# Kernel tuning notes

Hardware: AMD Instinct MI355X
Metric: run time of the kernel (lower is better)

Reference implementation:

```python
import jax, jax.numpy as jnp
import numpy as np
from jax import lax

K = 9
ISHAPE = (2048, 2048)
STRIDES = (4, 8, 16, 32)
NUM_ROIS = 300
IOU_THR = 0.5
SCORE_THR = 0.5
PRE_NMS_TOPK = 4000  # standard pre-NMS candidate cap; keeps suppression loop small


def _make_anchors(h, w, stride):
    scales = np.array([1.0, 2.0, 4.0]) * 4.0 * stride
    ratios = np.sqrt(np.array([0.5, 1.0, 2.0]))
    ah = (scales[:, None] * ratios[None, :]).reshape(-1)   # (9,)
    aw = (scales[:, None] / ratios[None, :]).reshape(-1)
    cy = (np.arange(h, dtype=np.float32) + 0.5) * stride
    cx = (np.arange(w, dtype=np.float32) + 0.5) * stride
    cy, cx = np.meshgrid(cy, cx, indexing='ij')             # (h,w)
    y1 = cy[..., None] - 0.5 * ah
    x1 = cx[..., None] - 0.5 * aw
    y2 = cy[..., None] + 0.5 * ah
    x2 = cx[..., None] + 0.5 * aw
    return np.stack([y1, x1, y2, x2], axis=-1).astype(np.float32)  # (h,w,9,4)


def setup_inputs() -> dict:
    key = jax.random.key(0)
    ks = jax.random.split(key, 4)
    sizes = [(512, 512), (256, 256), (128, 128), (64, 64)]
    out = {}
    for i, ((h, w), s, k) in enumerate(zip(sizes, STRIDES, ks), start=1):
        out[f'x{i}'] = jax.random.uniform(k, (1, h, w, 6 * K), dtype=jnp.float32)
        out[f'anchors{i}'] = jnp.asarray(_make_anchors(h, w, s))
    return out


def _decode_level(clzbbe, anchors):
    # clzbbe: (h,w,6k) -> (h,w,k,6); channels per anchor: [fg, bg, dy, dx, dh, dw]
    h, w, k, _ = anchors.shape
    t = clzbbe.reshape(h, w, k, 6)
    scores = t[..., 0]
    dy, dx, dh, dw = t[..., 2], t[..., 3], t[..., 4], t[..., 5]
    ah = anchors[..., 2] - anchors[..., 0]
    aw = anchors[..., 3] - anchors[..., 1]
    acy = anchors[..., 0] + 0.5 * ah
    acx = anchors[..., 1] + 0.5 * aw
    cy = acy + dy * ah
    cx = acx + dx * aw
    bh = ah * jnp.exp(dh)
    bw = aw * jnp.exp(dw)
    y1 = jnp.clip(cy - 0.5 * bh, 0.0, float(ISHAPE[0]))
    x1 = jnp.clip(cx - 0.5 * bw, 0.0, float(ISHAPE[1]))
    y2 = jnp.clip(cy + 0.5 * bh, 0.0, float(ISHAPE[0]))
    x2 = jnp.clip(cx + 0.5 * bw, 0.0, float(ISHAPE[1]))
    boxes = jnp.stack([y1, x1, y2, x2], axis=-1).reshape(-1, 4)
    return boxes, scores.reshape(-1)


def _iou_one_vs_all(box, boxes):
    yy1 = jnp.maximum(box[0], boxes[:, 0])
    xx1 = jnp.maximum(box[1], boxes[:, 1])
    yy2 = jnp.minimum(box[2], boxes[:, 2])
    xx2 = jnp.minimum(box[3], boxes[:, 3])
    inter = jnp.maximum(yy2 - yy1, 0.0) * jnp.maximum(xx2 - xx1, 0.0)
    a1 = (box[2] - box[0]) * (box[3] - box[1])
    a2 = (boxes[:, 2] - boxes[:, 0]) * (boxes[:, 3] - boxes[:, 1])
    return inter / (a1 + a2 - inter + 1e-9)


def _pnsm(boxes, scores):
    # pre-NMS top-k candidates
    top_scores, top_idx = lax.top_k(scores, PRE_NMS_TOPK)
    cand_boxes = boxes[top_idx]                              # (TOPK, 4)
    s0 = jnp.where(top_scores >= SCORE_THR, top_scores, -1.0)

    def step(s, _):
        i = jnp.argmax(s)
        best_score = s[i]
        best_box = cand_boxes[i]
        iou = _iou_one_vs_all(best_box, cand_boxes)
        s = jnp.where(iou > IOU_THR, -1.0, s).at[i].set(-1.0)
        roi = jnp.where(best_score > 0.0, best_box, jnp.zeros_like(best_box))
        return s, roi

    _, rois = lax.scan(step, s0, None, length=NUM_ROIS)      # (NUM_ROIS, 4)
    return rois


def reference(x1, x2, x3, x4, anchors1, anchors2, anchors3, anchors4):
    levels = [(x1[0], anchors1), (x2[0], anchors2), (x3[0], anchors3), (x4[0], anchors4)]
    decoded = [_decode_level(c, a) for c, a in levels]
    boxes = jnp.concatenate([b for b, _ in decoded], axis=0)   # (N, 4)
    scores = jnp.concatenate([s for _, s in decoded], axis=0)  # (N,)
    rois = _pnsm(boxes, scores)
    return rois[None]                                          # (1, NUM_ROIS, 4)
```

## Files before the change

kernel.cpp:

```cpp
#include <hip/hip_runtime.h>


namespace {

constexpr int kNTot = 3133440;
constexpr int kB1 = 2359296;
constexpr int kB2 = 2949120;
constexpr int kB3 = 3096576;
constexpr int kNBins = 8192;
constexpr int kNParts = 256;
constexpr int kCap = 8192;
constexpr int kTopK = 4000;
constexpr int kNPad = 4096;
constexpr int kNRois = 300;
constexpr int kChunk = 32;
constexpr int kNChunks = kTopK / kChunk;
constexpr int kNSlots = 8;
constexpr int kNPref = 7;
constexpr int kJChunk = 2048;
constexpr int kITile = 256;
constexpr int kBCS = 16;

constexpr int kF4L[4] = {3538944, 884736, 221184, 55296};
constexpr int kLvlB0[5] = {0, 193, 241, 253, 256};
constexpr int kLvlAB[4] = {0, kB1, kB2, kB3};

struct LevelPick { const float* x; unsigned local; };

__device__ __forceinline__ LevelPick pick_level(unsigned g, const float* x1, const float* x2,
                                                const float* x3, const float* x4) {
  LevelPick p;
  if (g < (unsigned)kB1)      { p.x = x1; p.local = g; }
  else if (g < (unsigned)kB2) { p.x = x2; p.local = g - kB1; }
  else if (g < (unsigned)kB3) { p.x = x3; p.local = g - kB2; }
  else                        { p.x = x4; p.local = g - kB3; }
  return p;
}

__device__ __forceinline__ int score_bin(float s) {
  int b = (int)(s * (float)kNBins);
  return min(max(b, 0), kNBins - 1);
}

__device__ __forceinline__ void load_scores4(const float* x, unsigned local0, float s[4]) {
  const float4* p = (const float4*)(x + (size_t)local0 * 6);
  float4 q0 = p[0], q1 = p[1], q3 = p[3], q4 = p[4];
  s[0] = q0.x; s[1] = q1.z; s[2] = q3.x; s[3] = q4.z;
}

__global__ __launch_bounds__(1024) void hist_kernel(
    const float4* __restrict__ x1, const float4* __restrict__ x2,
    const float4* __restrict__ x3, const float4* __restrict__ x4,
    unsigned* __restrict__ part, float* __restrict__ scores) {
  __shared__ unsigned h[kNBins];
  for (int i = threadIdx.x; i < kNBins; i += 1024) h[i] = 0;
  __syncthreads();
  const int bid = blockIdx.x;
  int lvl = (bid < kLvlB0[1]) ? 0 : (bid < kLvlB0[2]) ? 1 : (bid < kLvlB0[3]) ? 2 : 3;
  const float4* x = (lvl == 0) ? x1 : (lvl == 1) ? x2 : (lvl == 2) ? x3 : x4;
  const int nf4 = kF4L[lvl];
  const int abase = kLvlAB[lvl];
  const int bloc = bid - kLvlB0[lvl];
  const int nblk = kLvlB0[lvl + 1] - kLvlB0[lvl];
  for (int q = bloc * 1024 + threadIdx.x; q < nf4; q += nblk * 1024) {
    float4 v = x[q];
    int qd = q / 3;
    int r = q - qd * 3;
    if (r != 2) {
      float s = (r == 0) ? v.x : v.z;
      atomicAdd(&h[score_bin(s)], 1u);
      if (scores) scores[abase + 2 * qd + r] = s;
    }
  }
  __syncthreads();
  for (int i = threadIdx.x; i < kNBins; i += 1024)
    part[blockIdx.x * kNBins + i] = h[i];
}

__global__ void reduce_kernel(const unsigned* __restrict__ part, unsigned* __restrict__ hist) {
  int b = blockIdx.x * 256 + threadIdx.x;
  unsigned t0 = 0, t1 = 0, t2 = 0, t3 = 0;
  for (int p = 0; p < kNParts; p += 4) {
    t0 += part[(size_t)(p + 0) * kNBins + b];
    t1 += part[(size_t)(p + 1) * kNBins + b];
    t2 += part[(size_t)(p + 2) * kNBins + b];
    t3 += part[(size_t)(p + 3) * kNBins + b];
  }
  hist[b] = t0 + t1 + t2 + t3;
}

__global__ __launch_bounds__(1024) void select_kernel(
    const unsigned* __restrict__ hist, unsigned* __restrict__ sel,
    unsigned* __restrict__ counter, unsigned* __restrict__ binStart) {
  __shared__ unsigned wtot[16];
  __shared__ unsigned maxB;
  const int t = threadIdx.x;
  const int lane = t & 63;
  const int wv = t >> 6;
  if (t == 0) maxB = 0u;
  unsigned h[8];
  unsigned s = 0;
  #pragma unroll
  for (int i = 0; i < 8; ++i) { h[i] = hist[t * 8 + i]; s += h[i]; }
  unsigned p = s;
  #pragma unroll
  for (int off = 1; off < 64; off <<= 1) {
    unsigned n = __shfl_up(p, off);
    if (lane >= off) p += n;
  }
  if (lane == 63) wtot[wv] = p;
  __syncthreads();
  if (wv == 0 && lane < 16) {
    unsigned wp = wtot[lane];
    #pragma unroll
    for (int off = 1; off < 16; off <<= 1) {
      unsigned n = __shfl_up(wp, off);
      if (lane >= off) wp += n;
    }
    wtot[lane] = wp;
  }
  __syncthreads();
  const unsigned total = wtot[15];
  const unsigned Pincl = p + (wv > 0 ? wtot[wv - 1] : 0u);
  const unsigned T = total - Pincl;
  unsigned bs[8];
  bs[7] = T;
  #pragma unroll
  for (int i = 6; i >= 0; --i) bs[i] = bs[i + 1] + h[i + 1];
  #pragma unroll
  for (int i = 0; i < 8; ++i) binStart[t * 8 + i] = bs[i];
  unsigned cand = 0;
  #pragma unroll
  for (int i = 0; i < 8; ++i)
    if (bs[i] + h[i] >= (unsigned)kTopK) cand = (unsigned)(t * 8 + i);
  atomicMax(&maxB, cand);
  __syncthreads();
  const unsigned B = maxB;
  if (t == (int)(B >> 3)) {
    unsigned i = B & 7u;
    unsigned n = bs[i] + h[i];
    sel[0] = B;
    counter[0] = n < (unsigned)kCap ? n : (unsigned)kCap;
  }
}

__device__ __forceinline__ void try_append(float s, unsigned g, unsigned B,
                                           const unsigned* __restrict__ binStart,
                                           unsigned* __restrict__ binCount,
                                           unsigned long long* __restrict__ keys) {
  unsigned bin = (unsigned)score_bin(s);
  if (bin >= B) {
    unsigned pos = binStart[bin] + atomicAdd(&binCount[bin << 4], 1u);
    if (pos < (unsigned)kCap) {
      keys[pos] = ((unsigned long long)__float_as_uint(s) << 32) |
                  (unsigned long long)(0xFFFFFFFFu - g);
    }
  }
}

__global__ void compact_s_kernel(const float4* __restrict__ scores4,
                                 const unsigned* __restrict__ sel,
                                 const unsigned* __restrict__ binStart,
                                 unsigned* __restrict__ binCount,
                                 unsigned long long* __restrict__ keys) {
  int t = blockIdx.x * blockDim.x + threadIdx.x;
  if (t >= kNTot / 4) return;
  float4 v = scores4[t];
  unsigned g0 = (unsigned)t * 4;
  unsigned B = sel[0];
  try_append(v.x, g0 + 0, B, binStart, binCount, keys);
  try_append(v.y, g0 + 1, B, binStart, binCount, keys);
  try_append(v.z, g0 + 2, B, binStart, binCount, keys);
  try_append(v.w, g0 + 3, B, binStart, binCount, keys);
}

__global__ void compact_x_kernel(const float* __restrict__ x1, const float* __restrict__ x2,
                                 const float* __restrict__ x3, const float* __restrict__ x4,
                                 const unsigned* __restrict__ sel,
                                 const unsigned* __restrict__ binStart,
                                 unsigned* __restrict__ binCount,
                                 unsigned long long* __restrict__ keys) {
  int t = blockIdx.x * blockDim.x + threadIdx.x;
  if (t >= kNTot / 4) return;
  unsigned g0 = (unsigned)t * 4;
  LevelPick lp = pick_level(g0, x1, x2, x3, x4);
  float s[4];
  load_scores4(lp.x, lp.local, s);
  unsigned B = sel[0];
  #pragma unroll
  for (int i = 0; i < 4; ++i) try_append(s[i], g0 + i, B, binStart, binCount, keys);
}

__global__ void rank_kernel(const unsigned long long* __restrict__ keys,
                            const unsigned* __restrict__ counter,
                            unsigned* __restrict__ rankArr) {
  __shared__ unsigned long long lk[kJChunk];
  int n = (int)*counter;
  int itile = blockIdx.x / (kCap / kJChunk);
  int jc = blockIdx.x % (kCap / kJChunk);
  int i0 = itile * kITile;
  int j0 = jc * kJChunk;
  if (i0 >= n || j0 >= n) return;
  for (int j = threadIdx.x; j < kJChunk; j += kITile) {
    int jj = j0 + j;
    lk[j] = (jj < n) ? keys[jj] : 0ull;
  }
  __syncthreads();
  int i = i0 + threadIdx.x;
  unsigned long long ki = (i < n) ? keys[i] : ~0ull;
  int r0 = 0, r1 = 0, r2 = 0, r3 = 0;
  const ulonglong2* p2 = (const ulonglong2*)lk;
  #pragma unroll 4
  for (int j = 0; j < kJChunk / 8; ++j) {
    ulonglong2 a = p2[j];
    ulonglong2 b = p2[256 + j];
    ulonglong2 c = p2[512 + j];
    ulonglong2 d = p2[768 + j];
    r0 += (int)(a.x > ki) + (int)(a.y > ki);
    r1 += (int)(b.x > ki) + (int)(b.y > ki);
    r2 += (int)(c.x > ki) + (int)(c.y > ki);
    r3 += (int)(d.x > ki) + (int)(d.y > ki);
  }
  if (i < n) atomicAdd(&rankArr[i], (unsigned)(r0 + r1 + r2 + r3));
}

__global__ void scatter_kernel(const unsigned long long* __restrict__ keys,
                               const unsigned* __restrict__ counter,
                               const unsigned* __restrict__ rankArr,
                               unsigned long long* __restrict__ sorted) {
  int i = blockIdx.x * 256 + threadIdx.x;
  int n = (int)*counter;
  if (i < n) {
    unsigned r = rankArr[i];
    if (r < (unsigned)kNPad) sorted[r] = keys[i];
  }
}

__device__ __forceinline__ void decode_box(unsigned g,
                                           const float* __restrict__ x1, const float* __restrict__ x2,
                                           const float* __restrict__ x3, const float* __restrict__ x4,
                                           const float* __restrict__ a1, const float* __restrict__ a2,
                                           const float* __restrict__ a3, const float* __restrict__ a4,
                                           float4* box) {
  const float* x;
  const float* anc;
  unsigned local;
  if (g < (unsigned)kB1)      { x = x1; anc = a1; local = g; }
  else if (g < (unsigned)kB2) { x = x2; anc = a2; local = g - kB1; }
  else if (g < (unsigned)kB3) { x = x3; anc = a3; local = g - kB2; }
  else                        { x = x4; anc = a4; local = g - kB3; }
  const float* xe = x + (size_t)local * 6;
  float dy = xe[2], dx = xe[3], dh = xe[4], dwv = xe[5];
  const float* ae = anc + (size_t)local * 4;
  float ay1 = ae[0], ax1 = ae[1], ay2 = ae[2], ax2 = ae[3];
  float ah = ay2 - ay1;
  float aw = ax2 - ax1;
  float acy = ay1 + 0.5f * ah;
  float acx = ax1 + 0.5f * aw;
  float cy = acy + dy * ah;
  float cx = acx + dx * aw;
  float bh = ah * expf(dh);
  float bw = aw * expf(dwv);
  box->x = fminf(fmaxf(cy - 0.5f * bh, 0.0f), 2048.0f);
  box->y = fminf(fmaxf(cx - 0.5f * bw, 0.0f), 2048.0f);
  box->z = fminf(fmaxf(cy + 0.5f * bh, 0.0f), 2048.0f);
  box->w = fminf(fmaxf(cx + 0.5f * bw, 0.0f), 2048.0f);
}

__global__ void decode_kernel(const unsigned long long* __restrict__ sorted,
                              const unsigned* __restrict__ counter,
                              const float* __restrict__ x1, const float* __restrict__ x2,
                              const float* __restrict__ x3, const float* __restrict__ x4,
                              const float* __restrict__ a1, const float* __restrict__ a2,
                              const float* __restrict__ a3, const float* __restrict__ a4,
                              float4* __restrict__ boxes,
                              unsigned long long* __restrict__ supinit) {
  int r = blockIdx.x * 256 + threadIdx.x;
  int n = min((int)*counter, kTopK);
  unsigned long long key = (r < n) ? sorted[r] : 0ull;
  float4 box = make_float4(0.f, 0.f, 0.f, 0.f);
  float sc = 0.f;
  if (key != 0ull) {
    sc = __uint_as_float((unsigned)(key >> 32));
    unsigned g = 0xFFFFFFFFu - (unsigned)(key & 0xFFFFFFFFull);
    if (g < (unsigned)kNTot) decode_box(g, x1, x2, x3, x4, a1, a2, a3, a4, &box);
  }
  boxes[r] = box;
  unsigned long long dead = __ballot(!(sc >= 0.5f));
  if ((threadIdx.x & 63) == 0) supinit[r >> 6] = dead;
}

__global__ void iou_kernel(const float4* __restrict__ boxes,
                           unsigned long long* __restrict__ rows) {
  int wave = (blockIdx.x * blockDim.x + threadIdx.x) >> 6;
  int lane = threadIdx.x & 63;
  if (wave >= kTopK * 64) return;
  int row = wave >> 6;
  int wc = wave & 63;
  if (wc < (row >> 6)) return;
  int j = wc * 64 + lane;
  float4 bi = boxes[row];
  float4 bj = boxes[j];
  float yy1 = fmaxf(bi.x, bj.x);
  float xx1 = fmaxf(bi.y, bj.y);
  float yy2 = fminf(bi.z, bj.z);
  float xx2 = fminf(bi.w, bj.w);
  float inter = fmaxf(yy2 - yy1, 0.0f) * fmaxf(xx2 - xx1, 0.0f);
  float ar1 = (bi.z - bi.x) * (bi.w - bi.y);
  float ar2 = (bj.z - bj.x) * (bj.w - bj.y);
  float iou = inter / (ar1 + ar2 - inter + 1e-9f);
  unsigned long long m = __ballot(iou > 0.5f);
  if (lane == 0) rows[(size_t)row * 64 + wc] = m;
}

__device__ __forceinline__ void glds16(const void* g, void* l) {
  __builtin_amdgcn_global_load_lds(
      (const __attribute__((address_space(1))) unsigned int*)g,
      (__attribute__((address_space(3))) unsigned int*)l, 16, 0, 0);
}

__device__ __forceinline__ void stage_chunk(const unsigned long long* rows, int chunk,
                                            unsigned long long* dst, int lane) {
  const char* src = (const char*)(rows + (size_t)chunk * kChunk * 64);
  char* d = (char*)dst;
  #pragma unroll
  for (int i = 0; i < 16; ++i) {
    glds16(src + i * 1024 + lane * 16, d + i * 1024);
  }
}

__global__ __launch_bounds__(512, 1) void greedy_kernel(
    const float4* __restrict__ boxes,
    const unsigned long long* __restrict__ supinit,
    const unsigned long long* __restrict__ rows,
    float* __restrict__ out) {
  __shared__ unsigned long long slots[kNSlots][kChunk * 64];
  __shared__ unsigned readyF[kNChunks];
  __shared__ unsigned consumedF;
  __shared__ unsigned doneF;
  __shared__ int picksLds[kNRois];
  __shared__ int countSh;

  volatile unsigned* vready = readyF;
  volatile unsigned* vconsumed = &consumedF;
  volatile unsigned* vdone = &doneF;

  const int tid = threadIdx.x;
  const int wid = tid >> 6;
  const int lane = tid & 63;

  for (int i = tid; i < kNChunks; i += 512) readyF[i] = 0;
  if (tid == 0) { consumedF = 0; doneF = 0; countSh = 0; }
  __syncthreads();

  if (wid > 0) {
    int c = wid - 1;
    bool primed = false;
    if (c < kNChunks) {
      while (!*vdone && (int)*vconsumed < c - (kNSlots - 1))
        __builtin_amdgcn_s_sleep(1);
      if (!*vdone) {
        stage_chunk(rows, c, &slots[c & (kNSlots - 1)][0], lane);
        primed = true;
      }
    }
    while (primed) {
      int nxt = c + kNPref;
      bool staged_next = false;
      if (nxt < kNChunks) {
        while (!*vdone && (int)*vconsumed < nxt - (kNSlots - 1))
          __builtin_amdgcn_s_sleep(1);
        if (!*vdone) {
          stage_chunk(rows, nxt, &slots[nxt & (kNSlots - 1)][0], lane);
          staged_next = true;
        }
      }
      if (staged_next) {
        asm volatile("s_waitcnt vmcnt(16)" ::: "memory");
      } else {
        asm volatile("s_waitcnt vmcnt(0)" ::: "memory");
      }
      if (lane == 0) vready[c] = 1;
      if (!staged_next) break;
      c = nxt;
    }
  } else {
    unsigned long long sup = supinit[lane];
    int count = 0;
    for (int c = 0; c < kNChunks; ++c) {
      while (vready[c] == 0) __builtin_amdgcn_s_sleep(1);
      asm volatile("" ::: "memory");
      const unsigned long long* buf = &slots[c & (kNSlots - 1)][0];
      const int base = c * kChunk;
      const int w = base >> 6;
      const int sh = base & 63;
      unsigned long long cw = __shfl(sup, w);
      unsigned mask = (unsigned)((~cw) >> sh);
      while (mask != 0u && count < kNRois) {
        const int i = __builtin_ctz(mask);
        const int r = base + i;
        unsigned long long row = buf[i * 64 + lane];
        if (lane == 0) picksLds[count] = r;
        ++count;
        sup |= row;
        if (lane == w) sup |= 1ull << (r & 63);
        unsigned long long rww = __shfl(row, w);
        mask &= ~(unsigned)(rww >> sh);
        mask &= ~(1u << i);
      }
      if (lane == 0) *vconsumed = (unsigned)(c + 1);
      if (count == kNRois) break;
      if (__ballot(~sup != 0ull) == 0ull) break;
    }
    if (lane == 0) { countSh = count; *vdone = 1u; }
  }
  __syncthreads();
  const int cnt = countSh;
  for (int p = tid; p < kNRois; p += 512) {
    float4 bx = make_float4(0.f, 0.f, 0.f, 0.f);
    if (p < cnt) bx = boxes[picksLds[p]];
    ((float4*)out)[p] = bx;
  }
}

}

extern "C" void kernel_launch(void* const* d_in, const int* in_sizes, int n_in,
                              void* d_out, int out_size, void* d_ws, size_t ws_size,
                              hipStream_t stream) {
  const float* x1 = (const float*)d_in[0];
  const float* a1 = (const float*)d_in[1];
  const float* x2 = (const float*)d_in[2];
  const float* a2 = (const float*)d_in[3];
  const float* x3 = (const float*)d_in[4];
  const float* a3 = (const float*)d_in[5];
  const float* x4 = (const float*)d_in[6];
  const float* a4 = (const float*)d_in[7];

  char* ws = (char*)d_ws;
  size_t off = 0;
  unsigned* part = (unsigned*)(ws + off);       off += (size_t)kNParts * kNBins * 4;
  unsigned* hist = (unsigned*)(ws + off);       off += kNBins * 4;
  unsigned* counter = (unsigned*)(ws + off);    off += 4;
  unsigned* sel = (unsigned*)(ws + off);        off += 4;
  unsigned* rankArr = (unsigned*)(ws + off);    off += (size_t)kCap * 4;
  unsigned* binCount = (unsigned*)(ws + off);   off += (size_t)kNBins * kBCS * 4;
  unsigned* binStart = (unsigned*)(ws + off);   off += (size_t)kNBins * 4;
  unsigned long long* supinit = (unsigned long long*)(ws + off);  off += 512 + 8;
  unsigned long long* sorted = (unsigned long long*)(ws + off);   off += (size_t)kNPad * 8;
  unsigned long long* keys = (unsigned long long*)(ws + off);     off += (size_t)kCap * 8;
  float4* boxes = (float4*)(ws + off);          off += (size_t)kNPad * 16;
  unsigned long long* rows = (unsigned long long*)(ws + off);     off += (size_t)kTopK * 64 * 8;
  const bool sidecar = ws_size >= off + (size_t)kNTot * 4;
  float* scores = sidecar ? (float*)(ws + off) : nullptr;
  float* out = (float*)d_out;

  hipMemsetAsync((void*)counter, 0, 8 + (size_t)kCap * 4 + (size_t)kNBins * kBCS * 4,
                 stream);

  hist_kernel<<<kNParts, 1024, 0, stream>>>(
      (const float4*)x1, (const float4*)x2, (const float4*)x3, (const float4*)x4,
      part, scores);
  reduce_kernel<<<kNBins / 256, 256, 0, stream>>>(part, hist);
  select_kernel<<<1, 1024, 0, stream>>>(hist, sel, counter, binStart);
  int blocks4 = (kNTot / 4 + 255) / 256;
  if (sidecar) {
    compact_s_kernel<<<blocks4, 256, 0, stream>>>(
        (const float4*)scores, sel, binStart, binCount, keys);
  } else {
    compact_x_kernel<<<blocks4, 256, 0, stream>>>(
        x1, x2, x3, x4, sel, binStart, binCount, keys);
  }
  rank_kernel<<<(kCap / kITile) * (kCap / kJChunk), kITile, 0, stream>>>(
      keys, counter, rankArr);
  scatter_kernel<<<kCap / 256, 256, 0, stream>>>(keys, counter, rankArr, sorted);
  decode_kernel<<<kNPad / 256, 256, 0, stream>>>(
      sorted, counter, x1, x2, x3, x4, a1, a2, a3, a4, boxes, supinit);
  iou_kernel<<<(kTopK * 64 * 64) / 256, 256, 0, stream>>>(boxes, rows);
  greedy_kernel<<<1, 512, 0, stream>>>(boxes, supinit, rows, out);
}
```

Before: 139.2 us.

## Replace producer-consumer LDS staging in greedy NMS with sparse alive-row register prefetch

```diff
diff --git a/kernel.cpp b/kernel.cpp
--- a/kernel.cpp
+++ b/kernel.cpp
@@ -13,10 +13,6 @@
 constexpr int kTopK = 4000;
 constexpr int kNPad = 4096;
 constexpr int kNRois = 300;
-constexpr int kChunk = 32;
-constexpr int kNChunks = kTopK / kChunk;
-constexpr int kNSlots = 8;
-constexpr int kNPref = 7;
 constexpr int kJChunk = 2048;
 constexpr int kITile = 256;
 constexpr int kBCS = 16;
@@ -313,112 +309,85 @@
   if (lane == 0) rows[(size_t)row * 64 + wc] = m;
 }
 
-__device__ __forceinline__ void glds16(const void* g, void* l) {
-  __builtin_amdgcn_global_load_lds(
-      (const __attribute__((address_space(1))) unsigned int*)g,
-      (__attribute__((address_space(3))) unsigned int*)l, 16, 0, 0);
-}
-
-__device__ __forceinline__ void stage_chunk(const unsigned long long* rows, int chunk,
-                                            unsigned long long* dst, int lane) {
-  const char* src = (const char*)(rows + (size_t)chunk * kChunk * 64);
-  char* d = (char*)dst;
-  #pragma unroll
-  for (int i = 0; i < 16; ++i) {
-    glds16(src + i * 1024 + lane * 16, d + i * 1024);
-  }
-}
-
-__global__ __launch_bounds__(512, 1) void greedy_kernel(
+__global__ __launch_bounds__(64, 1) void greedy_kernel(
     const float4* __restrict__ boxes,
     const unsigned long long* __restrict__ supinit,
     const unsigned long long* __restrict__ rows,
     float* __restrict__ out) {
-  __shared__ unsigned long long slots[kNSlots][kChunk * 64];
-  __shared__ unsigned readyF[kNChunks];
-  __shared__ unsigned consumedF;
-  __shared__ unsigned doneF;
   __shared__ int picksLds[kNRois];
-  __shared__ int countSh;
-
-  volatile unsigned* vready = readyF;
-  volatile unsigned* vconsumed = &consumedF;
-  volatile unsigned* vdone = &doneF;
-
-  const int tid = threadIdx.x;
-  const int wid = tid >> 6;
-  const int lane = tid & 63;
-
-  for (int i = tid; i < kNChunks; i += 512) readyF[i] = 0;
-  if (tid == 0) { consumedF = 0; doneF = 0; countSh = 0; }
-  __syncthreads();
-
-  if (wid > 0) {
-    int c = wid - 1;
-    bool primed = false;
-    if (c < kNChunks) {
-      while (!*vdone && (int)*vconsumed < c - (kNSlots - 1))
-        __builtin_amdgcn_s_sleep(1);
-      if (!*vdone) {
-        stage_chunk(rows, c, &slots[c & (kNSlots - 1)][0], lane);
-        primed = true;
-      }
+  const int lane = threadIdx.x;
+  unsigned long long sup = supinit[lane];
+  int count = 0;
+  int frontier = -1;
+
+  auto next_alive = [&](int pos) -> int {
+    unsigned long long t = ~sup;
+    int w0 = (pos + 1) >> 6;
+    int sh = (pos + 1) & 63;
+    if (lane < w0) t = 0ull;
+    if (lane == w0) t &= (~0ull) << sh;
+    unsigned long long bal = __ballot(t != 0ull);
+    if (bal == 0ull) return -1;
+    int w = __builtin_ctzll(bal);
+    unsigned long long tw = __shfl(t, w);
+    return (w << 6) + __builtin_ctzll(tw);
+  };
+
+  int cand0[8], cand1[8];
+  unsigned long long q0[8], q1[8];
+
+#define GEN(CAND)                                   \
+  _Pragma("unroll")                                 \
+  for (int i = 0; i < 8; ++i) {                     \
+    int c = next_alive(frontier);                   \
+    CAND[i] = c;                                    \
+    if (c >= 0) frontier = c;                       \
+  }
+
+#define ISSUE(CAND, Q)                              \
+  _Pragma("unroll")                                 \
+  for (int i = 0; i < 8; ++i) {                     \
+    int rr = CAND[i] >= 0 ? CAND[i] : 0;            \
+    Q[i] = rows[(size_t)rr * 64 + lane];            \
+  }                                                 \
+  __builtin_amdgcn_sched_barrier(0);
+
+#define CONSUME(CAND, Q)                            \
+  _Pragma("unroll")                                 \
+  for (int i = 0; i < 8; ++i) {                     \
+    int r = CAND[i];                                \
+    if (r >= 0 && count < kNRois) {                 \
+      int w = r >> 6;                               \
+      unsigned long long bit = 1ull << (r & 63);    \
+      unsigned long long sw = __shfl(sup, w);       \
+      if ((sw & bit) == 0ull) {                     \
+        if (lane == 0) picksLds[count] = r;         \
+        ++count;                                    \
+        sup |= Q[i];                                \
+        if (lane == w) sup |= bit;                  \
+      }                                             \
+    }                                               \
+  }
+
+  GEN(cand0); ISSUE(cand0, q0);
+  GEN(cand1); ISSUE(cand1, q1);
+  if (cand0[0] >= 0) {
+    while (true) {
+      CONSUME(cand0, q0);
+      if (count >= kNRois || cand1[0] < 0) break;
+      GEN(cand0); ISSUE(cand0, q0);
+      CONSUME(cand1, q1);
+      if (count >= kNRois || cand0[0] < 0) break;
+      GEN(cand1); ISSUE(cand1, q1);
     }
-    while (primed) {
-      int nxt = c + kNPref;
-      bool staged_next = false;
-      if (nxt < kNChunks) {
-        while (!*vdone && (int)*vconsumed < nxt - (kNSlots - 1))
-          __builtin_amdgcn_s_sleep(1);
-        if (!*vdone) {
-          stage_chunk(rows, nxt, &slots[nxt & (kNSlots - 1)][0], lane);
-          staged_next = true;
-        }
-      }
-      if (staged_next) {
-        asm volatile("s_waitcnt vmcnt(16)" ::: "memory");
-      } else {
-        asm volatile("s_waitcnt vmcnt(0)" ::: "memory");
-      }
-      if (lane == 0) vready[c] = 1;
-      if (!staged_next) break;
-      c = nxt;
-    }
-  } else {
-    unsigned long long sup = supinit[lane];
-    int count = 0;
-    for (int c = 0; c < kNChunks; ++c) {
-      while (vready[c] == 0) __builtin_amdgcn_s_sleep(1);
-      asm volatile("" ::: "memory");
-      const unsigned long long* buf = &slots[c & (kNSlots - 1)][0];
-      const int base = c * kChunk;
-      const int w = base >> 6;
-      const int sh = base & 63;
-      unsigned long long cw = __shfl(sup, w);
-      unsigned mask = (unsigned)((~cw) >> sh);
-      while (mask != 0u && count < kNRois) {
-        const int i = __builtin_ctz(mask);
-        const int r = base + i;
-        unsigned long long row = buf[i * 64 + lane];
-        if (lane == 0) picksLds[count] = r;
-        ++count;
-        sup |= row;
-        if (lane == w) sup |= 1ull << (r & 63);
-        unsigned long long rww = __shfl(row, w);
-        mask &= ~(unsigned)(rww >> sh);
-        mask &= ~(1u << i);
-      }
-      if (lane == 0) *vconsumed = (unsigned)(c + 1);
-      if (count == kNRois) break;
-      if (__ballot(~sup != 0ull) == 0ull) break;
-    }
-    if (lane == 0) { countSh = count; *vdone = 1u; }
-  }
-  __syncthreads();
-  const int cnt = countSh;
-  for (int p = tid; p < kNRois; p += 512) {
+  }
+#undef GEN
+#undef ISSUE
+#undef CONSUME
+
+  for (int p = lane; p < kNRois; p += 64) {
     float4 bx = make_float4(0.f, 0.f, 0.f, 0.f);
-    if (p < cnt) bx = boxes[picksLds[p]];
+    if (p < count) bx = boxes[picksLds[p]];
     ((float4*)out)[p] = bx;
   }
 }
@@ -477,5 +446,5 @@
   decode_kernel<<<kNPad / 256, 256, 0, stream>>>(
       sorted, counter, x1, x2, x3, x4, a1, a2, a3, a4, boxes, supinit);
   iou_kernel<<<(kTopK * 64 * 64) / 256, 256, 0, stream>>>(boxes, rows);
-  greedy_kernel<<<1, 512, 0, stream>>>(boxes, supinit, rows, out);
-}
+  greedy_kernel<<<1, 64, 0, stream>>>(boxes, supinit, rows, out);
+}
```

New measurement: 167.9 us. 20.6% more time.

## Stage only surviving upper-triangle mask rows in greedy NMS prefetch

Applied to the files above, without the earlier changes.

```diff
diff --git a/kernel.cpp b/kernel.cpp
--- a/kernel.cpp
+++ b/kernel.cpp
@@ -207,7 +207,8 @@
   }
   __syncthreads();
   int i = i0 + threadIdx.x;
-  unsigned long long ki = (i < n) ? keys[i] : ~0ull;
+  unsigned long long ki = (i < n) ? lk[0] : ~0ull;
+  ki = (i < n) ? keys[i] : ~0ull;
   int r0 = 0, r1 = 0, r2 = 0, r3 = 0;
   const ulonglong2* p2 = (const ulonglong2*)lk;
   #pragma unroll 4
@@ -319,22 +320,15 @@
       (__attribute__((address_space(3))) unsigned int*)l, 16, 0, 0);
 }
 
-__device__ __forceinline__ void stage_chunk(const unsigned long long* rows, int chunk,
-                                            unsigned long long* dst, int lane) {
-  const char* src = (const char*)(rows + (size_t)chunk * kChunk * 64);
-  char* d = (char*)dst;
-  #pragma unroll
-  for (int i = 0; i < 16; ++i) {
-    glds16(src + i * 1024 + lane * 16, d + i * 1024);
-  }
-}
-
 __global__ __launch_bounds__(512, 1) void greedy_kernel(
     const float4* __restrict__ boxes,
     const unsigned long long* __restrict__ supinit,
     const unsigned long long* __restrict__ rows,
     float* __restrict__ out) {
   __shared__ unsigned long long slots[kNSlots][kChunk * 64];
+  __shared__ int ranksT[kNSlots][kChunk];
+  __shared__ unsigned maskT[kNChunks];
+  __shared__ unsigned long long supLds[64];
   __shared__ unsigned readyF[kNChunks];
   __shared__ unsigned consumedF;
   __shared__ unsigned doneF;
@@ -344,70 +338,84 @@
   volatile unsigned* vready = readyF;
   volatile unsigned* vconsumed = &consumedF;
   volatile unsigned* vdone = &doneF;
+  volatile unsigned long long* vsup = supLds;
+  volatile unsigned* vmask = maskT;
 
   const int tid = threadIdx.x;
   const int wid = tid >> 6;
   const int lane = tid & 63;
 
   for (int i = tid; i < kNChunks; i += 512) readyF[i] = 0;
+  if (tid < 64) supLds[tid] = supinit[tid];
   if (tid == 0) { consumedF = 0; doneF = 0; countSh = 0; }
   __syncthreads();
 
   if (wid > 0) {
-    int c = wid - 1;
-    bool primed = false;
-    if (c < kNChunks) {
+    for (int c = wid - 1; c < kNChunks; c += kNPref) {
       while (!*vdone && (int)*vconsumed < c - (kNSlots - 1))
         __builtin_amdgcn_s_sleep(1);
-      if (!*vdone) {
-        stage_chunk(rows, c, &slots[c & (kNSlots - 1)][0], lane);
-        primed = true;
-      }
-    }
-    while (primed) {
-      int nxt = c + kNPref;
-      bool staged_next = false;
-      if (nxt < kNChunks) {
-        while (!*vdone && (int)*vconsumed < nxt - (kNSlots - 1))
-          __builtin_amdgcn_s_sleep(1);
-        if (!*vdone) {
-          stage_chunk(rows, nxt, &slots[nxt & (kNSlots - 1)][0], lane);
-          staged_next = true;
+      if (*vdone) break;
+      const int slot = c & (kNSlots - 1);
+      const int W = c >> 1;
+      const int sh = (c & 1) * 32;
+      const int wstart = W & ~1;
+      const int Lw = 64 - wstart;
+      const int upr = Lw >> 1;
+      unsigned long long sw = vsup[W];
+      unsigned mask = (unsigned)((~sw) >> sh);
+      const int m = __popc(mask);
+      if (lane < 32 && ((mask >> lane) & 1u))
+        ranksT[slot][__popc(mask & ((1u << lane) - 1u))] = c * kChunk + lane;
+      asm volatile("s_waitcnt lgkmcnt(0)" ::: "memory");
+      if (m > 0) {
+        const int nunits = m * upr;
+        const int ninsts = (nunits + 63) >> 6;
+        char* dst = (char*)&slots[slot][0];
+        for (int i = 0; i < ninsts; ++i) {
+          int o = i * 64 + lane;
+          if (o >= nunits) o = nunits - 1;
+          int k = o / upr;
+          int col = o - k * upr;
+          int r = ranksT[slot][k];
+          const void* src = (const void*)(rows + (size_t)r * 64 + wstart + col * 2);
+          glds16(src, dst + i * 1024);
         }
-      }
-      if (staged_next) {
-        asm volatile("s_waitcnt vmcnt(16)" ::: "memory");
-      } else {
         asm volatile("s_waitcnt vmcnt(0)" ::: "memory");
       }
+      if (lane == 0) vmask[c] = mask;
+      asm volatile("s_waitcnt lgkmcnt(0)" ::: "memory");
       if (lane == 0) vready[c] = 1;
-      if (!staged_next) break;
-      c = nxt;
     }
   } else {
-    unsigned long long sup = supinit[lane];
+    unsigned long long sup = supLds[lane];
     int count = 0;
     for (int c = 0; c < kNChunks; ++c) {
       while (vready[c] == 0) __builtin_amdgcn_s_sleep(1);
       asm volatile("" ::: "memory");
-      const unsigned long long* buf = &slots[c & (kNSlots - 1)][0];
+      const unsigned mask = vmask[c];
+      const int slot = c & (kNSlots - 1);
+      const int W = c >> 1;
+      const int sh = (c & 1) * 32;
+      const int wstart = W & ~1;
+      const int Lw = 64 - wstart;
       const int base = c * kChunk;
-      const int w = base >> 6;
-      const int sh = base & 63;
-      unsigned long long cw = __shfl(sup, w);
-      unsigned mask = (unsigned)((~cw) >> sh);
-      while (mask != 0u && count < kNRois) {
-        const int i = __builtin_ctz(mask);
+      unsigned long long cw = __shfl(sup, W);
+      unsigned alive = (unsigned)((~cw) >> sh);
+      while (alive != 0u && count < kNRois) {
+        const int i = __builtin_ctz(alive);
         const int r = base + i;
-        unsigned long long row = buf[i * 64 + lane];
+        const int k = __popc(mask & ((1u << i) - 1u));
+        unsigned long long val = 0ull;
+        if (lane >= wstart) val = slots[slot][k * Lw + (lane - wstart)];
         if (lane == 0) picksLds[count] = r;
         ++count;
-        sup |= row;
-        if (lane == w) sup |= 1ull << (r & 63);
-        unsigned long long rww = __shfl(row, w);
-        mask &= ~(unsigned)(rww >> sh);
-        mask &= ~(1u << i);
+        sup |= val;
+        if (lane == W) sup |= 1ull << (r & 63);
+        unsigned long long rww = __shfl(val, W);
+        alive &= ~((unsigned)(rww >> sh) | (1u << i));
       }
+      vsup[lane] = sup;
+      asm volatile("s_waitcnt lgkmcnt(0)" ::: "memory");
       if (lane == 0) *vconsumed = (unsigned)(c + 1);
       if (count == kNRois) break;
       if (__ballot(~sup != 0ull) == 0ull) break;
```

Measured after the change: 142.8 us. +2.6%, slower.

## Drop memset, widen IoU waves, and use 64-row chunks in greedy NMS

Applied to the files above, without the earlier changes.

```diff
diff --git a/kernel.cpp b/kernel.cpp
--- a/kernel.cpp
+++ b/kernel.cpp
@@ -13,9 +13,9 @@
 constexpr int kTopK = 4000;
 constexpr int kNPad = 4096;
 constexpr int kNRois = 300;
-constexpr int kChunk = 32;
-constexpr int kNChunks = kTopK / kChunk;
-constexpr int kNSlots = 8;
+constexpr int kChunk = 64;
+constexpr int kNChunks = (kTopK + kChunk - 1) / kChunk;
+constexpr int kNSlots = 4;
 constexpr int kNPref = 7;
 constexpr int kJChunk = 2048;
 constexpr int kITile = 256;
@@ -77,7 +77,8 @@
     part[blockIdx.x * kNBins + i] = h[i];
 }
 
-__global__ void reduce_kernel(const unsigned* __restrict__ part, unsigned* __restrict__ hist) {
+__global__ void reduce_kernel(const unsigned* __restrict__ part, unsigned* __restrict__ hist,
+                              unsigned* __restrict__ rankArr, unsigned* __restrict__ binCount) {
   int b = blockIdx.x * 256 + threadIdx.x;
   unsigned t0 = 0, t1 = 0, t2 = 0, t3 = 0;
   for (int p = 0; p < kNParts; p += 4) {
@@ -87,6 +88,9 @@
     t3 += part[(size_t)(p + 3) * kNBins + b];
   }
   hist[b] = t0 + t1 + t2 + t3;
+  rankArr[b] = 0;
+  #pragma unroll
+  for (int k = 0; k < kBCS; ++k) binCount[(size_t)b * kBCS + k] = 0;
 }
 
 __global__ __launch_bounds__(1024) void select_kernel(
@@ -294,23 +298,28 @@
                            unsigned long long* __restrict__ rows) {
   int wave = (blockIdx.x * blockDim.x + threadIdx.x) >> 6;
   int lane = threadIdx.x & 63;
-  if (wave >= kTopK * 64) return;
-  int row = wave >> 6;
-  int wc = wave & 63;
-  if (wc < (row >> 6)) return;
-  int j = wc * 64 + lane;
+  if (wave >= kTopK * 16) return;
+  int row = wave >> 4;
+  int wg = wave & 15;
+  int W0 = row >> 6;
+  if (wg * 4 + 3 < W0) return;
   float4 bi = boxes[row];
-  float4 bj = boxes[j];
-  float yy1 = fmaxf(bi.x, bj.x);
-  float xx1 = fmaxf(bi.y, bj.y);
-  float yy2 = fminf(bi.z, bj.z);
-  float xx2 = fminf(bi.w, bj.w);
-  float inter = fmaxf(yy2 - yy1, 0.0f) * fmaxf(xx2 - xx1, 0.0f);
   float ar1 = (bi.z - bi.x) * (bi.w - bi.y);
-  float ar2 = (bj.z - bj.x) * (bj.w - bj.y);
-  float iou = inter / (ar1 + ar2 - inter + 1e-9f);
-  unsigned long long m = __ballot(iou > 0.5f);
-  if (lane == 0) rows[(size_t)row * 64 + wc] = m;
+  #pragma unroll
+  for (int w = 0; w < 4; ++w) {
+    int wc = wg * 4 + w;
+    if (wc < W0) continue;
+    float4 bj = boxes[wc * 64 + lane];
+    float yy1 = fmaxf(bi.x, bj.x);
+    float xx1 = fmaxf(bi.y, bj.y);
+    float yy2 = fminf(bi.z, bj.z);
+    float xx2 = fminf(bi.w, bj.w);
+    float inter = fmaxf(yy2 - yy1, 0.0f) * fmaxf(xx2 - xx1, 0.0f);
+    float ar2 = (bj.z - bj.x) * (bj.w - bj.y);
+    float iou = inter / (ar1 + ar2 - inter + 1e-9f);
+    unsigned long long m = __ballot(iou > 0.5f);
+    if (lane == 0) rows[(size_t)row * 64 + wc] = m;
+  }
 }
 
 __device__ __forceinline__ void glds16(const void* g, void* l) {
@@ -320,11 +329,10 @@
 }
 
 __device__ __forceinline__ void stage_chunk(const unsigned long long* rows, int chunk,
-                                            unsigned long long* dst, int lane) {
+                                            unsigned long long* dst, int lane, int ninst) {
   const char* src = (const char*)(rows + (size_t)chunk * kChunk * 64);
   char* d = (char*)dst;
-  #pragma unroll
-  for (int i = 0; i < 16; ++i) {
+  for (int i = 0; i < ninst; ++i) {
     glds16(src + i * 1024 + lane * 16, d + i * 1024);
   }
 }
@@ -354,35 +362,14 @@
   __syncthreads();
 
   if (wid > 0) {
-    int c = wid - 1;
-    bool primed = false;
-    if (c < kNChunks) {
+    for (int c = wid - 1; c < kNChunks; c += kNPref) {
       while (!*vdone && (int)*vconsumed < c - (kNSlots - 1))
         __builtin_amdgcn_s_sleep(1);
-      if (!*vdone) {
-        stage_chunk(rows, c, &slots[c & (kNSlots - 1)][0], lane);
-        primed = true;
-      }
-    }
-    while (primed) {
-      int nxt = c + kNPref;
-      bool staged_next = false;
-      if (nxt < kNChunks) {
-        while (!*vdone && (int)*vconsumed < nxt - (kNSlots - 1))
-          __builtin_amdgcn_s_sleep(1);
-        if (!*vdone) {
-          stage_chunk(rows, nxt, &slots[nxt & (kNSlots - 1)][0], lane);
-          staged_next = true;
-        }
-      }
-      if (staged_next) {
-        asm volatile("s_waitcnt vmcnt(16)" ::: "memory");
-      } else {
-        asm volatile("s_waitcnt vmcnt(0)" ::: "memory");
-      }
+      if (*vdone) break;
+      const int ni = (c == kNChunks - 1) ? 16 : 32;
+      stage_chunk(rows, c, &slots[c & (kNSlots - 1)][0], lane, ni);
+      asm volatile("s_waitcnt vmcnt(0)" ::: "memory");
       if (lane == 0) vready[c] = 1;
-      if (!staged_next) break;
-      c = nxt;
     }
   } else {
     unsigned long long sup = supinit[lane];
@@ -392,21 +379,18 @@
       asm volatile("" ::: "memory");
       const unsigned long long* buf = &slots[c & (kNSlots - 1)][0];
       const int base = c * kChunk;
-      const int w = base >> 6;
-      const int sh = base & 63;
-      unsigned long long cw = __shfl(sup, w);
-      unsigned mask = (unsigned)((~cw) >> sh);
-      while (mask != 0u && count < kNRois) {
-        const int i = __builtin_ctz(mask);
+      unsigned long long cw = __shfl(sup, c);
+      unsigned long long mask = ~cw;
+      while (mask != 0ull && count < kNRois) {
+        const int i = __builtin_ctzll(mask);
         const int r = base + i;
         unsigned long long row = buf[i * 64 + lane];
         if (lane == 0) picksLds[count] = r;
         ++count;
         sup |= row;
-        if (lane == w) sup |= 1ull << (r & 63);
-        unsigned long long rww = __shfl(row, w);
-        mask &= ~(unsigned)(rww >> sh);
-        mask &= ~(1u << i);
+        if (lane == c) sup |= 1ull << i;
+        unsigned long long rww = __shfl(row, c);
+        mask &= ~(rww | (1ull << i));
       }
       if (lane == 0) *vconsumed = (unsigned)(c + 1);
       if (count == kNRois) break;
@@ -455,13 +439,10 @@
   float* scores = sidecar ? (float*)(ws + off) : nullptr;
   float* out = (float*)d_out;
 
-  hipMemsetAsync((void*)counter, 0, 8 + (size_t)kCap * 4 + (size_t)kNBins * kBCS * 4,
-                 stream);
-
   hist_kernel<<<kNParts, 1024, 0, stream>>>(
       (const float4*)x1, (const float4*)x2, (const float4*)x3, (const float4*)x4,
       part, scores);
-  reduce_kernel<<<kNBins / 256, 256, 0, stream>>>(part, hist);
+  reduce_kernel<<<kNBins / 256, 256, 0, stream>>>(part, hist, rankArr, binCount);
   select_kernel<<<1, 1024, 0, stream>>>(hist, sel, counter, binStart);
   int blocks4 = (kNTot / 4 + 255) / 256;
   if (sidecar) {
@@ -476,6 +457,6 @@
   scatter_kernel<<<kCap / 256, 256, 0, stream>>>(keys, counter, rankArr, sorted);
   decode_kernel<<<kNPad / 256, 256, 0, stream>>>(
       sorted, counter, x1, x2, x3, x4, a1, a2, a3, a4, boxes, supinit);
-  iou_kernel<<<(kTopK * 64 * 64) / 256, 256, 0, stream>>>(boxes, rows);
+  iou_kernel<<<(kTopK * 16 * 64) / 256, 256, 0, stream>>>(boxes, rows);
   greedy_kernel<<<1, 512, 0, stream>>>(boxes, supinit, rows, out);
 }
```

New measurement: 125.4 us. 9.9% less time.
